# Kernel tuning notes

Hardware: AMD Instinct MI355X
Metric: run time of the kernel (lower is better)

Reference implementation:

```python
import jax, jax.numpy as jnp
import numpy as np

HEADS = 4
DIM_HEAD = 32
DIM = 128
HIDDEN = HEADS * DIM_HEAD  # 128


def setup_inputs() -> dict:
    key = jax.random.key(0)
    k1, k2, k3, k4 = jax.random.split(key, 4)
    B, C, H, W = 8, DIM, 128, 128
    x = jax.random.normal(k1, (B, C, H, W), dtype=jnp.float32)
    # 1x1 conv weights stored as [out_ch, in_ch] (kernel dims squeezed)
    w_qkv = jax.random.normal(k2, (3 * HIDDEN, DIM), dtype=jnp.float32) * (1.0 / np.sqrt(DIM))
    w_out = jax.random.normal(k3, (DIM, HIDDEN), dtype=jnp.float32) * (1.0 / np.sqrt(HIDDEN))
    b_out = jax.random.normal(k4, (DIM,), dtype=jnp.float32) * 0.01
    return {"x": x, "w_qkv": w_qkv, "w_out": w_out, "b_out": b_out}


def reference(x, w_qkv, w_out, b_out):
    b, c, h, w = x.shape
    n = h * w
    # 1x1 conv == per-pixel matmul over channels
    qkv = jnp.einsum('bchw,oc->bohw', x, w_qkv)            # [b, 3*HIDDEN, h, w]
    # channel layout: (qkv, heads, dim_head)
    qkv = qkv.reshape(b, 3, HEADS, DIM_HEAD, n)            # [b, 3, H, d, n]
    q, k, v = qkv[:, 0], qkv[:, 1], qkv[:, 2]
    k = jax.nn.softmax(k, axis=-1)                         # softmax over spatial n
    context = jnp.einsum('bhdn,bhen->bhde', k, v)          # [b, H, d, d] (tiny)
    out = jnp.einsum('bhde,bhdn->bhen', context, q)        # [b, H, d, n]
    out = out.reshape(b, HIDDEN, h, w)
    y = jnp.einsum('bchw,oc->bohw', out, w_out) + b_out[None, :, None, None]
    return y
```

## Files before the change

kernel.cpp:

```cpp
#include <hip/hip_runtime.h>
#include <math.h>

#define C_ 128
#define N_ 16384

#define WS_Z    0
#define WS_CTX  1024
#define WS_BMAT 33792
#define WS_A    164864
#define WS_PCTX 295936
#define WS_PZ   (WS_PCTX + 1024*4096)
#define WS_END  (WS_PZ + 512*128)

typedef __attribute__((ext_vector_type(8))) short bf16x8;
typedef __attribute__((ext_vector_type(4))) float f32x4;
typedef __attribute__((ext_vector_type(4))) unsigned int u32x4;
typedef __attribute__((ext_vector_type(2))) unsigned int u32x2;

__device__ __forceinline__ unsigned int pkbf(float a, float b) {
  unsigned int r;
  asm("v_cvt_pk_bf16_f32 %0, %1, %2" : "=v"(r) : "v"(a), "v"(b));
  return r;
}

__device__ __forceinline__ bf16x8 make_frag(float4 u, float4 v) {
  u32x4 q = {pkbf(u.x, u.y), pkbf(u.z, u.w), pkbf(v.x, v.y), pkbf(v.z, v.w)};
  return *(bf16x8*)&q;
}

__device__ __forceinline__ bf16x8 lds_frag16(const unsigned short* p) {
  u32x4 q = *(const u32x4*)p;
  return *(bf16x8*)&q;
}

__device__ __forceinline__ void load4(const float* p, float* o) {
  float4 v = *(const float4*)p;
  o[0] = v.x; o[1] = v.y; o[2] = v.z; o[3] = v.w;
}

template<bool ATOMIC>
__global__ __launch_bounds__(512, 2) void k1_kv_ctx(const float* __restrict__ x,
                                                    const float* __restrict__ wqkv,
                                                    float* __restrict__ ws) {
  __shared__ __attribute__((aligned(16))) unsigned short xs[64][136];
  __shared__ __attribute__((aligned(16))) unsigned short ekv[2][128][72];
  const int tid  = threadIdx.x;
  const int wave = tid >> 6;
  const int l15  = tid & 15;
  const int l4   = (tid >> 4) & 3;
  const int b    = blockIdx.y;
  const int j    = blockIdx.x;
  const int h    = wave & 3;
  const int t    = wave >> 2;
  const int kvrow0 = h * 32 + t * 128;
  const float* xb = x + (size_t)b * ((size_t)C_ * N_);

  const int sn4 = tid & 15;
  const int scq = tid >> 4;

  bf16x8 wf[2][4];
  #pragma unroll
  for (int mi = 0; mi < 2; ++mi)
    #pragma unroll
    for (int ki = 0; ki < 4; ++ki) {
      const float* p = wqkv + (size_t)(128 + kvrow0 + mi * 16 + l15) * C_ + ki * 32 + l4 * 8;
      wf[mi][ki] = make_frag(*(const float4*)p, *(const float4*)(p + 4));
    }

  {
    float va[4][4];
    #pragma unroll
    for (int r = 0; r < 4; ++r)
      load4(xb + (size_t)(scq * 4 + r) * N_ + j * 256 + sn4 * 4, va[r]);
    #pragma unroll
    for (int i = 0; i < 4; ++i) {
      u32x2 w = {pkbf(va[0][i], va[1][i]), pkbf(va[2][i], va[3][i])};
      *(u32x2*)&xs[sn4 * 4 + i][scq * 4] = w;
    }
  }
  __syncthreads();

  const f32x4 z4 = {0.f, 0.f, 0.f, 0.f};
  f32x4 ctxacc[2][2];
  #pragma unroll
  for (int i = 0; i < 2; ++i)
    #pragma unroll
    for (int jj = 0; jj < 2; ++jj) ctxacc[i][jj] = z4;
  float zacc[2] = {0.f, 0.f};

  for (int st = 0; st < 4; ++st) {
    float pf[4][4];
    if (st < 3) {
      const int nbn = j * 256 + (st + 1) * 64;
      #pragma unroll
      for (int r = 0; r < 4; ++r)
        load4(xb + (size_t)(scq * 4 + r) * N_ + nbn + sn4 * 4, pf[r]);
    }

    #pragma unroll
    for (int half = 0; half < 2; ++half) {
      f32x4 acc[2][2];
      #pragma unroll
      for (int a = 0; a < 2; ++a)
        #pragma unroll
        for (int m = 0; m < 2; ++m) acc[a][m] = z4;
      #pragma unroll
      for (int ki = 0; ki < 4; ++ki) {
        bf16x8 bfr[2];
        #pragma unroll
        for (int ni2 = 0; ni2 < 2; ++ni2)
          bfr[ni2] = lds_frag16(&xs[half * 32 + ni2 * 16 + l15][ki * 32 + l4 * 8]);
        #pragma unroll
        for (int ni2 = 0; ni2 < 2; ++ni2)
          #pragma unroll
          for (int mi = 0; mi < 2; ++mi)
            acc[ni2][mi] = __builtin_amdgcn_mfma_f32_16x16x32_bf16(
                bfr[ni2], wf[mi][ki], acc[ni2][mi], 0, 0, 0);
      }
      #pragma unroll
      for (int ni2 = 0; ni2 < 2; ++ni2)
        #pragma unroll
        for (int mi = 0; mi < 2; ++mi) {
          float e0, e1, e2, e3;
          if (t == 0) {
            e0 = __expf(acc[ni2][mi][0]); e1 = __expf(acc[ni2][mi][1]);
            e2 = __expf(acc[ni2][mi][2]); e3 = __expf(acc[ni2][mi][3]);
            zacc[mi] += (e0 + e1) + (e2 + e3);
          } else {
            e0 = acc[ni2][mi][0]; e1 = acc[ni2][mi][1];
            e2 = acc[ni2][mi][2]; e3 = acc[ni2][mi][3];
          }
          u32x2 w = {pkbf(e0, e1), pkbf(e2, e3)};
          *(u32x2*)&ekv[t][h * 32 + mi * 16 + l15][(half * 2 + ni2) * 16 + l4 * 4] = w;
        }
    }
    __syncthreads();

    {
      bf16x8 af2[2], bv2[2];
      #pragma unroll
      for (int m2 = 0; m2 < 2; ++m2)
        af2[m2] = lds_frag16(&ekv[0][h * 32 + m2 * 16 + l15][t * 32 + l4 * 8]);
      #pragma unroll
      for (int n2 = 0; n2 < 2; ++n2)
        bv2[n2] = lds_frag16(&ekv[1][h * 32 + n2 * 16 + l15][t * 32 + l4 * 8]);
      #pragma unroll
      for (int m2 = 0; m2 < 2; ++m2)
        #pragma unroll
        for (int n2 = 0; n2 < 2; ++n2)
          ctxacc[m2][n2] = __builtin_amdgcn_mfma_f32_16x16x32_bf16(
              af2[m2], bv2[n2], ctxacc[m2][n2], 0, 0, 0);
    }

    if (st < 3) {
      #pragma unroll
      for (int i = 0; i < 4; ++i) {
        u32x2 w = {pkbf(pf[0][i], pf[1][i]), pkbf(pf[2][i], pf[3][i])};
        *(u32x2*)&xs[sn4 * 4 + i][scq * 4] = w;
      }
    }
    __syncthreads();
  }

  if (!ATOMIC) {
    float* ps = ws + WS_PCTX + (size_t)((b * 64 + j) * 2 + t) * 4096 + h * 1024;
    #pragma unroll
    for (int m2 = 0; m2 < 2; ++m2)
      #pragma unroll
      for (int n2 = 0; n2 < 2; ++n2)
        #pragma unroll
        for (int r = 0; r < 4; ++r)
          ps[(m2 * 16 + l4 * 4 + r) * 32 + n2 * 16 + l15] = ctxacc[m2][n2][r];
  } else {
    float* ctx = ws + WS_CTX + (size_t)(b * 4 + h) * 1024;
    #pragma unroll
    for (int m2 = 0; m2 < 2; ++m2)
      #pragma unroll
      for (int n2 = 0; n2 < 2; ++n2)
        #pragma unroll
        for (int r = 0; r < 4; ++r)
          atomicAdd(&ctx[(m2 * 16 + l4 * 4 + r) * 32 + n2 * 16 + l15],
                    ctxacc[m2][n2][r]);
  }
  if (t == 0) {
    #pragma unroll
    for (int mi = 0; mi < 2; ++mi) {
      float z = zacc[mi];
      z += __shfl_xor(z, 16);
      z += __shfl_xor(z, 32);
      if ((tid & 48) == 0) {
        int row = h * 32 + mi * 16 + l15;
        if (!ATOMIC)
          ws[WS_PZ + (size_t)(b * 64 + j) * 128 + row] = z;
        else
          atomicAdd(&ws[WS_Z + b * 128 + row], z);
      }
    }
  }
}

__global__ __launch_bounds__(256) void k1b(float* __restrict__ ws) {
  const int tid = threadIdx.x;
  const int eq = blockIdx.x;
  const int h  = blockIdx.y;
  const int b  = blockIdx.z;
  const int el = eq * 256 + tid;
  const float* p = ws + WS_PCTX + (size_t)(b * 128) * 4096 + h * 1024 + el;
  float s = 0.f;
  #pragma unroll 8
  for (int jj = 0; jj < 128; ++jj) s += p[(size_t)jj * 4096];
  ws[WS_CTX + (size_t)(b * 4 + h) * 1024 + el] = s;
  if (eq == 0 && tid < 32) {
    const float* pz = ws + WS_PZ + (size_t)(b * 64) * 128 + h * 32 + tid;
    float z = 0.f;
    #pragma unroll 8
    for (int jj = 0; jj < 64; ++jj) z += pz[(size_t)jj * 128];
    ws[WS_Z + b * 128 + h * 32 + tid] = z;
  }
}

__global__ __launch_bounds__(256) void k2a(const float* __restrict__ w_qkv,
                                           float* __restrict__ ws) {
  __shared__ float cn[32][33];
  __shared__ float wqs[32][128];
  const int tid = threadIdx.x;
  const int h = blockIdx.x, b = blockIdx.y;
  const float* Z   = ws + WS_Z + b * 128 + h * 32;
  const float* ctx = ws + WS_CTX + ((b * 4 + h) * 32) * 32;

  for (int k = 0; k < 4; ++k) {
    int idx = tid + k * 256;
    int d = idx >> 5, e = idx & 31;
    cn[d][e] = ctx[d * 32 + e] / Z[d];
  }
  for (int k = 0; k < 4; ++k) {
    int idx = tid + k * 256;
    int d = idx >> 5, f4 = idx & 31;
    *(float4*)&wqs[d][f4 * 4] = *(const float4*)(w_qkv + (h * 32 + d) * 128 + f4 * 4);
  }
  __syncthreads();

  const int e = tid >> 3, cs = (tid & 7) * 16;
  float s[16];
  #pragma unroll
  for (int jj = 0; jj < 16; ++jj) s[jj] = 0.f;
  for (int d = 0; d < 32; ++d) {
    float v = cn[d][e];
    #pragma unroll
    for (int jj = 0; jj < 16; ++jj) s[jj] = fmaf(v, wqs[d][cs + jj], s[jj]);
  }
  float* Bm = ws + WS_BMAT + ((size_t)b * 128 + h * 32 + e) * 128;
  #pragma unroll
  for (int jj = 0; jj < 16; ++jj) Bm[cs + jj] = s[jj];
}

__global__ __launch_bounds__(256) void k2b(const float* __restrict__ w_out,
                                           float* __restrict__ ws) {
  __shared__ float bs[128][128];
  __shared__ float wos[32][128];
  const int tid = threadIdx.x;
  const int oq = blockIdx.x, b = blockIdx.y;
  const float* Bm = ws + WS_BMAT + (size_t)b * 128 * 128;

  for (int k = 0; k < 16; ++k) {
    int idx = tid + k * 256;
    int r = idx >> 5, f4 = idx & 31;
    *(float4*)&bs[r][f4 * 4] = *(const float4*)(Bm + r * 128 + f4 * 4);
  }
  for (int k = 0; k < 4; ++k) {
    int idx = tid + k * 256;
    int r = idx >> 5, f4 = idx & 31;
    *(float4*)&wos[r][f4 * 4] = *(const float4*)(w_out + (oq * 32 + r) * 128 + f4 * 4);
  }
  __syncthreads();

  const int ol = tid >> 3, cq = (tid & 7) * 16;
  float s[16];
  #pragma unroll
  for (int jj = 0; jj < 16; ++jj) s[jj] = 0.f;
  for (int eg = 0; eg < 128; ++eg) {
    float w = wos[ol][eg];
    #pragma unroll
    for (int jj = 0; jj < 16; ++jj) s[jj] = fmaf(w, bs[eg][cq + jj], s[jj]);
  }
  float* A = ws + WS_A + ((size_t)b * 128 + oq * 32 + ol) * 128;
  #pragma unroll
  for (int jj = 0; jj < 16; ++jj) A[cq + jj] = s[jj];
}

__global__ __launch_bounds__(256, 4) void k3(const float* __restrict__ x,
                                             const float* __restrict__ bout,
                                             const float* __restrict__ ws,
                                             float* __restrict__ y) {
  __shared__ __attribute__((aligned(16))) unsigned short xs2[2][64][136];
  const int tid  = threadIdx.x;
  const int wave = tid >> 6;
  const int l15  = tid & 15;
  const int l4   = (tid >> 4) & 3;
  const int b    = blockIdx.y;
  const int n0   = blockIdx.x * 128;
  const float* xb = x + (size_t)b * ((size_t)C_ * N_);
  const float* A  = ws + WS_A + (size_t)b * 128 * 128;

  bf16x8 af[2][4];
  #pragma unroll
  for (int mi = 0; mi < 2; ++mi)
    #pragma unroll
    for (int ki = 0; ki < 4; ++ki) {
      const float* p = A + (size_t)(wave * 32 + mi * 16 + l15) * 128 + ki * 32 + l4 * 8;
      af[mi][ki] = make_frag(*(const float4*)p, *(const float4*)(p + 4));
    }
  float bias[2];
  #pragma unroll
  for (int mi = 0; mi < 2; ++mi) bias[mi] = bout[wave * 32 + mi * 16 + l15];

  #pragma unroll
  for (int it = 0; it < 2; ++it) {
    int idx = tid + it * 256;
    int n4 = idx & 15, cq = idx >> 4;
    float va[4][4];
    #pragma unroll
    for (int r = 0; r < 4; ++r)
      load4(xb + (size_t)(cq * 4 + r) * N_ + n0 + n4 * 4, va[r]);
    #pragma unroll
    for (int i = 0; i < 4; ++i) {
      u32x2 w = {pkbf(va[0][i], va[1][i]), pkbf(va[2][i], va[3][i])};
      *(u32x2*)&xs2[0][n4 * 4 + i][cq * 4] = w;
    }
  }
  __syncthreads();

  const f32x4 z4 = {0.f, 0.f, 0.f, 0.f};
  float* yb = y + (size_t)b * ((size_t)128 * N_);

  #pragma unroll
  for (int st = 0; st < 2; ++st) {
    const int nb = n0 + st * 64;
    f32x4 acc[4][2];
    #pragma unroll
    for (int ni = 0; ni < 4; ++ni)
      #pragma unroll
      for (int mi = 0; mi < 2; ++mi) acc[ni][mi] = z4;
    #pragma unroll
    for (int ki = 0; ki < 4; ++ki) {
      bf16x8 bfr[4];
      #pragma unroll
      for (int ni = 0; ni < 4; ++ni)
        bfr[ni] = lds_frag16(&xs2[st][ni * 16 + l15][ki * 32 + l4 * 8]);
      #pragma unroll
      for (int ni = 0; ni < 4; ++ni)
        #pragma unroll
        for (int mi = 0; mi < 2; ++mi)
          acc[ni][mi] = __builtin_amdgcn_mfma_f32_16x16x32_bf16(
              bfr[ni], af[mi][ki], acc[ni][mi], 0, 0, 0);
    }

    if (st == 0) {
      #pragma unroll
      for (int it = 0; it < 2; ++it) {
        int idx = tid + it * 256;
        int n4 = idx & 15, cq = idx >> 4;
        float va[4][4];
        #pragma unroll
        for (int r = 0; r < 4; ++r)
          load4(xb + (size_t)(cq * 4 + r) * N_ + n0 + 64 + n4 * 4, va[r]);
        #pragma unroll
        for (int i = 0; i < 4; ++i) {
          u32x2 w = {pkbf(va[0][i], va[1][i]), pkbf(va[2][i], va[3][i])};
          *(u32x2*)&xs2[1][n4 * 4 + i][cq * 4] = w;
        }
      }
    }

    #pragma unroll
    for (int ni = 0; ni < 4; ++ni)
      #pragma unroll
      for (int mi = 0; mi < 2; ++mi) {
        float4 o;
        o.x = acc[ni][mi][0] + bias[mi];
        o.y = acc[ni][mi][1] + bias[mi];
        o.z = acc[ni][mi][2] + bias[mi];
        o.w = acc[ni][mi][3] + bias[mi];
        *(float4*)(yb + (size_t)(wave * 32 + mi * 16 + l15) * N_ + nb + ni * 16 + l4 * 4) = o;
      }

    if (st == 0) __syncthreads();
  }
}

extern "C" void kernel_launch(void* const* d_in, const int* in_sizes, int n_in,
                              void* d_out, int out_size, void* d_ws, size_t ws_size,
                              hipStream_t stream) {
  const float* x     = (const float*)d_in[0];
  const float* w_qkv = (const float*)d_in[1];
  const float* w_out = (const float*)d_in[2];
  const float* b_out = (const float*)d_in[3];
  float* y  = (float*)d_out;
  float* ws = (float*)d_ws;

  const bool partial = ws_size >= (size_t)WS_END * sizeof(float);
  if (partial) {
    k1_kv_ctx<false><<<dim3(64, 8), 512, 0, stream>>>(x, w_qkv, ws);
    k1b<<<dim3(4, 4, 8), 256, 0, stream>>>(ws);
  } else {
    hipMemsetAsync(ws, 0, (1024 + 32768) * sizeof(float), stream);
    k1_kv_ctx<true><<<dim3(64, 8), 512, 0, stream>>>(x, w_qkv, ws);
  }
  k2a<<<dim3(4, 8), 256, 0, stream>>>(w_qkv, ws);
  k2b<<<dim3(4, 8), 256, 0, stream>>>(w_out, ws);
  k3<<<dim3(128, 8), 256, 0, stream>>>(x, b_out, ws, y);
}
```

Baseline: 79.89 us.

## Swizzle bf16 LDS tiles, fuse k2a/k2b into one kernel, relax k3 occupancy

Adds an XOR swizzle on the 272-byte-stride bf16 LDS tiles in k1 and k3 to cut bank conflicts on the 16-byte MFMA fragment reads and on the transposed writes. Merges k2a and k2b into a single kernel that builds the B matrix in shared memory, removing one launch and the global round trip through WS_BMAT. Each k2 block now recomputes all four heads' B rows redundantly. Also lowers k3's launch_bounds min-blocks hint from 4 to 2, which lets the compiler use more registers at the possible cost of occupancy.

```diff
diff --git a/kernel.cpp b/kernel.cpp
--- a/kernel.cpp
+++ b/kernel.cpp
@@ -36,6 +36,10 @@
 __device__ __forceinline__ void load4(const float* p, float* o) {
   float4 v = *(const float4*)p;
   o[0] = v.x; o[1] = v.y; o[2] = v.z; o[3] = v.w;
+}
+
+__device__ __forceinline__ void* xsa(void* base, int row, int col_bytes) {
+  return (void*)((char*)base + row * 272 + (col_bytes ^ (((row >> 2) & 7) << 4)));
 }
 
 template<bool ATOMIC>
@@ -75,7 +79,7 @@
     #pragma unroll
     for (int i = 0; i < 4; ++i) {
       u32x2 w = {pkbf(va[0][i], va[1][i]), pkbf(va[2][i], va[3][i])};
-      *(u32x2*)&xs[sn4 * 4 + i][scq * 4] = w;
+      *(u32x2*)xsa(xs, sn4 * 4 + i, scq * 8) = w;
     }
   }
   __syncthreads();
@@ -109,7 +113,8 @@
         bf16x8 bfr[2];
         #pragma unroll
         for (int ni2 = 0; ni2 < 2; ++ni2)
-          bfr[ni2] = lds_frag16(&xs[half * 32 + ni2 * 16 + l15][ki * 32 + l4 * 8]);
+          bfr[ni2] = lds_frag16((const unsigned short*)
+              xsa(xs, half * 32 + ni2 * 16 + l15, ki * 64 + l4 * 16));
         #pragma unroll
         for (int ni2 = 0; ni2 < 2; ++ni2)
           #pragma unroll
@@ -156,7 +161,7 @@
       #pragma unroll
       for (int i = 0; i < 4; ++i) {
         u32x2 w = {pkbf(pf[0][i], pf[1][i]), pkbf(pf[2][i], pf[3][i])};
-        *(u32x2*)&xs[sn4 * 4 + i][scq * 4] = w;
+        *(u32x2*)xsa(xs, sn4 * 4 + i, scq * 8) = w;
       }
     }
     __syncthreads();
@@ -219,61 +224,54 @@
   }
 }
 
-__global__ __launch_bounds__(256) void k2a(const float* __restrict__ w_qkv,
-                                           float* __restrict__ ws) {
+__global__ __launch_bounds__(256) void k2(const float* __restrict__ w_qkv,
+                                          const float* __restrict__ w_out,
+                                          float* __restrict__ ws) {
+  __shared__ float bs[128][132];
+  __shared__ float wqs[32][128];
+  __shared__ float wos[32][132];
   __shared__ float cn[32][33];
-  __shared__ float wqs[32][128];
-  const int tid = threadIdx.x;
-  const int h = blockIdx.x, b = blockIdx.y;
-  const float* Z   = ws + WS_Z + b * 128 + h * 32;
-  const float* ctx = ws + WS_CTX + ((b * 4 + h) * 32) * 32;
-
-  for (int k = 0; k < 4; ++k) {
-    int idx = tid + k * 256;
-    int d = idx >> 5, e = idx & 31;
-    cn[d][e] = ctx[d * 32 + e] / Z[d];
-  }
-  for (int k = 0; k < 4; ++k) {
-    int idx = tid + k * 256;
-    int d = idx >> 5, f4 = idx & 31;
-    *(float4*)&wqs[d][f4 * 4] = *(const float4*)(w_qkv + (h * 32 + d) * 128 + f4 * 4);
-  }
-  __syncthreads();
-
-  const int e = tid >> 3, cs = (tid & 7) * 16;
-  float s[16];
-  #pragma unroll
-  for (int jj = 0; jj < 16; ++jj) s[jj] = 0.f;
-  for (int d = 0; d < 32; ++d) {
-    float v = cn[d][e];
-    #pragma unroll
-    for (int jj = 0; jj < 16; ++jj) s[jj] = fmaf(v, wqs[d][cs + jj], s[jj]);
-  }
-  float* Bm = ws + WS_BMAT + ((size_t)b * 128 + h * 32 + e) * 128;
-  #pragma unroll
-  for (int jj = 0; jj < 16; ++jj) Bm[cs + jj] = s[jj];
-}
-
-__global__ __launch_bounds__(256) void k2b(const float* __restrict__ w_out,
-                                           float* __restrict__ ws) {
-  __shared__ float bs[128][128];
-  __shared__ float wos[32][128];
   const int tid = threadIdx.x;
   const int oq = blockIdx.x, b = blockIdx.y;
-  const float* Bm = ws + WS_BMAT + (size_t)b * 128 * 128;
-
-  for (int k = 0; k < 16; ++k) {
-    int idx = tid + k * 256;
-    int r = idx >> 5, f4 = idx & 31;
-    *(float4*)&bs[r][f4 * 4] = *(const float4*)(Bm + r * 128 + f4 * 4);
-  }
+
+  for (int h = 0; h < 4; ++h) {
+    if (h) __syncthreads();
+    const float* Z   = ws + WS_Z + b * 128 + h * 32;
+    const float* ctx = ws + WS_CTX + ((b * 4 + h) * 32) * 32;
+    #pragma unroll
+    for (int k = 0; k < 4; ++k) {
+      int idx = tid + k * 256;
+      int d = idx >> 5, e = idx & 31;
+      cn[d][e] = ctx[d * 32 + e] / Z[d];
+    }
+    #pragma unroll
+    for (int k = 0; k < 4; ++k) {
+      int idx = tid + k * 256;
+      int d = idx >> 5, f4 = idx & 31;
+      *(float4*)&wqs[d][f4 * 4] = *(const float4*)(w_qkv + (h * 32 + d) * 128 + f4 * 4);
+    }
+    __syncthreads();
+    const int e = tid >> 3, cs = (tid & 7) * 16;
+    float s[16];
+    #pragma unroll
+    for (int jj = 0; jj < 16; ++jj) s[jj] = 0.f;
+    for (int d = 0; d < 32; ++d) {
+      float v = cn[d][e];
+      #pragma unroll
+      for (int jj = 0; jj < 16; ++jj) s[jj] = fmaf(v, wqs[d][cs + jj], s[jj]);
+    }
+    #pragma unroll
+    for (int jj = 0; jj < 16; ++jj) bs[h * 32 + e][cs + jj] = s[jj];
+  }
+
+  __syncthreads();
+  #pragma unroll
   for (int k = 0; k < 4; ++k) {
     int idx = tid + k * 256;
     int r = idx >> 5, f4 = idx & 31;
     *(float4*)&wos[r][f4 * 4] = *(const float4*)(w_out + (oq * 32 + r) * 128 + f4 * 4);
   }
   __syncthreads();
-
   const int ol = tid >> 3, cq = (tid & 7) * 16;
   float s[16];
   #pragma unroll
@@ -288,7 +286,7 @@
   for (int jj = 0; jj < 16; ++jj) A[cq + jj] = s[jj];
 }
 
-__global__ __launch_bounds__(256, 4) void k3(const float* __restrict__ x,
+__global__ __launch_bounds__(256, 2) void k3(const float* __restrict__ x,
                                              const float* __restrict__ bout,
                                              const float* __restrict__ ws,
                                              float* __restrict__ y) {
@@ -325,7 +323,7 @@
     #pragma unroll
     for (int i = 0; i < 4; ++i) {
       u32x2 w = {pkbf(va[0][i], va[1][i]), pkbf(va[2][i], va[3][i])};
-      *(u32x2*)&xs2[0][n4 * 4 + i][cq * 4] = w;
+      *(u32x2*)xsa(&xs2[0][0][0], n4 * 4 + i, cq * 8) = w;
     }
   }
   __syncthreads();
@@ -346,7 +344,8 @@
       bf16x8 bfr[4];
       #pragma unroll
       for (int ni = 0; ni < 4; ++ni)
-        bfr[ni] = lds_frag16(&xs2[st][ni * 16 + l15][ki * 32 + l4 * 8]);
+        bfr[ni] = lds_frag16((const unsigned short*)
+            xsa(&xs2[st][0][0], ni * 16 + l15, ki * 64 + l4 * 16));
       #pragma unroll
       for (int ni = 0; ni < 4; ++ni)
         #pragma unroll
@@ -367,7 +366,7 @@
         #pragma unroll
         for (int i = 0; i < 4; ++i) {
           u32x2 w = {pkbf(va[0][i], va[1][i]), pkbf(va[2][i], va[3][i])};
-          *(u32x2*)&xs2[1][n4 * 4 + i][cq * 4] = w;
+          *(u32x2*)xsa(&xs2[1][0][0], n4 * 4 + i, cq * 8) = w;
         }
       }
     }
@@ -406,7 +405,6 @@
     hipMemsetAsync(ws, 0, (1024 + 32768) * sizeof(float), stream);
     k1_kv_ctx<true><<<dim3(64, 8), 512, 0, stream>>>(x, w_qkv, ws);
   }
-  k2a<<<dim3(4, 8), 256, 0, stream>>>(w_qkv, ws);
-  k2b<<<dim3(4, 8), 256, 0, stream>>>(w_out, ws);
+  k2<<<dim3(4, 8), 256, 0, stream>>>(w_qkv, w_out, ws);
   k3<<<dim3(128, 8), 256, 0, stream>>>(x, b_out, ws, y);
 }
```

New measurement: 84.40 us. 5.6% more time.
